# Optimization experiments

Measured on AMD Instinct MI355X. Metric: run time of the kernel, lower is better.

The kernel has to match this reference:

```python
import jax, jax.numpy as jnp
import numpy as np

T, N = 24, 2048
INPUT_DIM, HIDDEN, MEDIATE, SOCIAL, OUT_DIM = 2, 64, 128, 64, 2
N_SIZE = 2
CELL = 0.3
T_OBS, T_PRED = 9, 19
WIN = (N_SIZE + 1) ** 2  # (N_size+1)^2 = 9 window cells


def _social_pool(h, coords, mask):
    """Faithful social pooling for N_size=2, grid_cell_size=0.3.

    torch builds a dynamic grid, scatter-adds every agent's h into its cell,
    then gathers grid[int(x-R):int(x+R), int(y-R):int(y+R)] per agent.
    With R=0.3 and integer positions >= 4 (guaranteed by the margin), that
    slice is exactly the single cell (x-1, y-1), broadcast over the 3x3
    window. We compute it as a pairwise match without materializing a grid.
    Runs under torch.no_grad() -> stop_gradient.
    """
    margin = 2 * N_SIZE * CELL
    lt = jnp.stack([coords[:, 0].min(), coords[:, 1].min()]) - margin
    p = jnp.floor((coords - lt) / CELL).astype(jnp.int32)            # [N,2]
    p = p * mask.astype(jnp.int32)[:, None]                          # masked agents -> cell (0,0)
    q = p - 1                                                        # gathered cell per agent
    match = (p[None, :, 0] == q[:, None, 0]) & (p[None, :, 1] == q[:, None, 1])  # [i,j]
    cell_val = match.astype(h.dtype) @ h                             # [N,hidden] scatter-add + gather
    Hf = jnp.tile(cell_val, (1, WIN)) * mask[:, None]                # broadcast over 3x3 window, flat
    return jax.lax.stop_gradient(Hf)


def _forward(X, part_masks, all_h_t, all_c_t, Y, W_in, b_in, W_soc, b_soc,
             W_ih, W_hh, b_ih, b_hh, W_out, b_out, T_obs, T_pred):
    relu = jax.nn.relu  # dropout_prob = 0 -> Phi == ReLU

    def lstm(z, h, c):
        g = z @ W_ih.T + b_ih + h @ W_hh.T + b_hh
        i, f, gg, o = jnp.split(g, 4, axis=1)
        c = jax.nn.sigmoid(f) * c + jax.nn.sigmoid(i) * jnp.tanh(gg)
        h = jax.nn.sigmoid(o) * jnp.tanh(c)
        return h, c

    def cell_out(r, h, c, coords, m):
        Hf = _social_pool(h, coords, m)
        e = relu(Hf @ W_soc.T + b_soc)
        z = jnp.concatenate([r, e], axis=1)
        h, c = lstm(z, h, c)
        out = (h @ W_out.T + b_out) * m[:, None]
        return h, c, out

    def step_obs(carry, inp):
        h, c = carry
        x, m = inp
        r = relu(x @ W_in.T + b_in)
        h, c, out = cell_out(r, h, c, x, m)
        return (h, c), out

    (h, c), outs_obs = jax.lax.scan(
        step_obs, (all_h_t, all_c_t), (X[:T_obs + 1], part_masks[:T_obs + 1]))

    def step_pred(carry, inp):
        h, c, last_pt, prev_out = carry
        x, m = inp
        r = relu(last_pt @ W_in.T + b_in)
        h, c, out = cell_out(r, h, c, x, m)
        # torch: last_point = outputs[frame_idx - 1] AFTER the frame runs
        return (h, c, prev_out, out), out

    carry0 = (h, c, X[T_obs + 1], outs_obs[-1])
    _, outs_pred = jax.lax.scan(
        step_pred, carry0, (X[T_obs + 1:T_pred + 1], part_masks[T_obs + 1:T_pred + 1]))

    tail = jnp.zeros((X.shape[0] - T_pred - 1, X.shape[1], OUT_DIM), X.dtype)
    return jnp.concatenate([outs_obs, outs_pred, tail], axis=0)


def setup_inputs() -> dict:
    key = jax.random.key(0)
    ks = jax.random.split(key, 13)

    def lin(kw, kb, out_d, in_d):  # torch nn.Linear default init
        lim = 1.0 / float(np.sqrt(in_d))
        W = jax.random.uniform(kw, (out_d, in_d), minval=-lim, maxval=lim, dtype=jnp.float32)
        b = jax.random.uniform(kb, (out_d,), minval=-lim, maxval=lim, dtype=jnp.float32)
        return W, b

    W_in, b_in = lin(ks[0], ks[1], MEDIATE, INPUT_DIM)
    W_soc, b_soc = lin(ks[2], ks[3], SOCIAL, WIN * HIDDEN)
    W_ih, b_ih = lin(ks[4], ks[5], 4 * HIDDEN, MEDIATE + SOCIAL)
    W_hh, b_hh = lin(ks[6], ks[7], 4 * HIDDEN, HIDDEN)
    W_out, b_out = lin(ks[8], ks[9], OUT_DIM, HIDDEN)

    X = jax.random.normal(ks[10], (T, N, INPUT_DIM), dtype=jnp.float32) * 10.0  # meter-scale coords
    part_masks = (jax.random.uniform(ks[11], (T, N)) < 0.9).astype(jnp.float32)  # binary presence mask
    Y = jax.random.normal(ks[12], (T, N, INPUT_DIM), dtype=jnp.float32)  # unused by forward
    all_h_t = jnp.zeros((N, HIDDEN), jnp.float32)
    all_c_t = jnp.zeros((N, HIDDEN), jnp.float32)

    return {"X": X, "part_masks": part_masks, "all_h_t": all_h_t, "all_c_t": all_c_t,
            "Y": Y, "T_obs": T_OBS, "T_pred": T_PRED,
            "W_in": W_in, "b_in": b_in, "W_soc": W_soc, "b_soc": b_soc,
            "W_ih": W_ih, "W_hh": W_hh, "b_ih": b_ih, "b_hh": b_hh,
            "W_out": W_out, "b_out": b_out}


def reference(X, part_masks, all_h_t, all_c_t, Y, T_obs, T_pred,
              W_in, b_in, W_soc, b_soc, W_ih, W_hh, b_ih, b_hh, W_out, b_out):
    return _forward(X, part_masks, all_h_t, all_c_t, Y, W_in, b_in, W_soc, b_soc,
                    W_ih, W_hh, b_ih, b_hh, W_out, b_out, int(T_obs), int(T_pred))
```

## Files before the change

kernel.cpp:

```cpp
#include <hip/hip_runtime.h>
#include <math.h>


#define N_AG   2048
#define STEPS  20
#define CAP    12
#define NSRV   21
#define MAGIC  0x13572468

typedef short short8 __attribute__((ext_vector_type(8)));
typedef float f32x4  __attribute__((ext_vector_type(4)));
union FU { uint4 q; short8 v; };

__device__ __forceinline__ void pack8(const float* v, uint4& hq, uint4& lq) {
    unsigned uh[4], ul[4];
    #pragma unroll
    for (int w = 0; w < 4; w++) {
        float v0 = v[2 * w], v1 = v[2 * w + 1];
        unsigned h;
        asm("v_cvt_pk_bf16_f32 %0, %1, %2" : "=v"(h) : "v"(v0), "v"(v1));
        float f0 = __uint_as_float(h << 16);
        float f1 = __uint_as_float(h & 0xffff0000u);
        float r0 = v0 - f0, r1 = v1 - f1;
        unsigned l;
        asm("v_cvt_pk_bf16_f32 %0, %1, %2" : "=v"(l) : "v"(r0), "v"(r1));
        uh[w] = h; ul[w] = l;
    }
    hq = make_uint4(uh[0], uh[1], uh[2], uh[3]);
    lq = make_uint4(ul[0], ul[1], ul[2], ul[3]);
}

__device__ __forceinline__ int khash(int k) {
    return (int)(((unsigned)k * 2654435761u) >> 21);
}

__device__ __forceinline__ float fsigm(float x) {
    return __builtin_amdgcn_rcpf(1.f + __expf(-x));
}
__device__ __forceinline__ float ftanh(float x) {
    float e = __expf(2.f * x);
    return 1.f - 2.f * __builtin_amdgcn_rcpf(e + 1.f);
}

__device__ __forceinline__ void bar_lds() {
    asm volatile("s_waitcnt lgkmcnt(0)\n\ts_barrier" ::: "memory");
}

__device__ __forceinline__ void ast(int* p_, int v) {
    __hip_atomic_store(p_, v, __ATOMIC_RELAXED, __HIP_MEMORY_SCOPE_AGENT);
}
__device__ __forceinline__ void astf(float* p_, float v) {
    __hip_atomic_store(p_, v, __ATOMIC_RELAXED, __HIP_MEMORY_SCOPE_AGENT);
}
__device__ __forceinline__ unsigned long long aldu64(const unsigned long long* p_) {
    return __hip_atomic_load(p_, __ATOMIC_RELAXED, __HIP_MEMORY_SCOPE_AGENT);
}

struct KP {
    const float *X, *masks, *h_in, *c_in;
    const float *Win, *bin, *Wsoc, *bsoc, *Wih, *Whh, *bih, *bhh, *Wout, *bout;
    float *Wef;
    int *mcnt, *midx, *need, *flags;
    float *out;
    unsigned long long *hist;
};

__global__ __launch_bounds__(512, 1) void k_all(KP p)
{
    __shared__ __align__(16) uint4 zshq[544];
    __shared__ float gbuf[16][260];
    __shared__ float gbuf2[8][260];
    __shared__ __align__(16) float cvs[8][68];
    __shared__ __align__(16) float hs[8][68];
    __shared__ __align__(16) float sWefP[64 * 66];
    __shared__ float2 sWinP[16 * 17];
    __shared__ float sBinP[16 * 9];
    __shared__ float sX[11][8][2];
    __shared__ float sMask[STEPS][8];
    __shared__ int   sCnt[STEPS][8];
    __shared__ int   sNeed[19][8];
    __shared__ int   sMidx[STEPS][8][CAP];
    __shared__ float sBsoc[64], sBc[256], sWout[128], sBout[2];
    __shared__ uint4 sE0h[8], sE0l[8];
    __shared__ int kk[N_AG];
    __shared__ int head[N_AG];
    __shared__ int nxt[N_AG];
    __shared__ float red[512];

    const int tid = threadIdx.x;
    const int bxg = blockIdx.x;

    if (bxg < NSRV) {
        const int sb = bxg;
        {
            int lo = sb * 780;
            int hi = (sb == NSRV - 1) ? 16384 : lo + 780;
            for (int i = lo + tid; i < hi; i += 512)
                p.out[20 * N_AG * 2 + i] = 0.f;
        }
        if (sb == 20) {
            for (int i = tid; i < 4096; i += 512) {
                int s = i >> 6, k = i & 63;
                float a = 0.f;
                #pragma unroll
                for (int w = 0; w < 9; w++) a += p.Wsoc[s * 576 + w * 64 + k];
                astf(&p.Wef[i], a);
            }
            __syncthreads();
            if (tid == 0) ast(&p.flags[20], MAGIC);
        } else {
            const int t = sb;
            const float* Xt = p.X + t * N_AG * 2;

            float mnx = 1e30f, mny = 1e30f;
            for (int i = tid; i < N_AG; i += 512) {
                mnx = fminf(mnx, Xt[2 * i]);
                mny = fminf(mny, Xt[2 * i + 1]);
            }
            red[tid] = mnx; __syncthreads();
            for (int s = 256; s > 0; s >>= 1) { if (tid < s) red[tid] = fminf(red[tid], red[tid + s]); __syncthreads(); }
            float ltx = red[0]; __syncthreads();
            red[tid] = mny; __syncthreads();
            for (int s = 256; s > 0; s >>= 1) { if (tid < s) red[tid] = fminf(red[tid], red[tid + s]); __syncthreads(); }
            float lty = red[0]; __syncthreads();
            ltx -= 1.2f;
            lty -= 1.2f;

            for (int i = tid; i < N_AG; i += 512) {
                float m = p.masks[t * N_AG + i];
                int px = (int)floorf((Xt[2 * i]     - ltx) / 0.3f);
                int py = (int)floorf((Xt[2 * i + 1] - lty) / 0.3f);
                int im = (int)m;
                px *= im; py *= im;
                kk[i] = px * 65536 + py;
                head[i] = -1;
                if (t >= 1) ast(&p.need[(t - 1) * N_AG + i], 0);
            }
            __syncthreads();
            for (int j = tid; j < N_AG; j += 512) {
                int kj = kk[j];
                if (kj != 0) nxt[j] = atomicExch(&head[khash(kj)], j);
            }
            __syncthreads();
            for (int i = tid; i < N_AG; i += 512) {
                int ki = kk[i];
                int cnt = 0;
                int base = (t * N_AG + i) * CAP;
                if (ki != 0) {
                    int tkey = ki - 65537;
                    int lst[CAP];
                    for (int j = head[khash(tkey)]; j >= 0; j = nxt[j]) {
                        if (kk[j] == tkey) { if (cnt < CAP) lst[cnt] = j; cnt++; }
                    }
                    if (cnt > CAP) cnt = CAP;
                    for (int a = 1; a < cnt; a++) {
                        int v = lst[a]; int b = a - 1;
                        while (b >= 0 && lst[b] > v) { lst[b + 1] = lst[b]; b--; }
                        lst[b + 1] = v;
                    }
                    for (int a = 0; a < cnt; a++) {
                        ast(&p.midx[base + a], lst[a]);
                        if (t >= 1) ast(&p.need[(t - 1) * N_AG + lst[a]], 1);
                    }
                }
                ast(&p.mcnt[t * N_AG + i], cnt);
            }
            __syncthreads();
            if (tid == 0) ast(&p.flags[t], MAGIC);
        }
    }

    const int wbase = bxg * 8;
    const int wv    = tid >> 6, lane = tid & 63;
    const int mA    = lane & 15, quad = lane >> 4;
    const int nt0   = 2 * wv;
    const int w     = wv;

    if (tid < 256) sBc[tid] = p.bih[tid] + p.bhh[tid];
    if (tid < 128) {
        sWout[tid] = p.Wout[tid];
        int c = tid;
        sWinP[(c >> 3) * 17 + (c & 7)] = make_float2(p.Win[2 * c], p.Win[2 * c + 1]);
        sBinP[(c >> 3) * 9 + (c & 7)] = p.bin[c];
    }
    if (tid < 64) sBsoc[tid] = p.bsoc[tid];
    if (tid < 2)  sBout[tid] = p.bout[tid];
    if (tid < 8) {
        float v[8];
        #pragma unroll
        for (int j = 0; j < 8; j++) v[j] = fmaxf(p.bsoc[tid * 8 + j], 0.f);
        pack8(v, sE0h[tid], sE0l[tid]);
    }
    if (tid < 176) { int tt = tid / 16, r = tid % 16;
                     sX[tt][r >> 1][r & 1] = p.X[tt * (N_AG * 2) + (wbase + (r >> 1)) * 2 + (r & 1)]; }
    if (tid < 160) { int tt = tid / 8, m2 = tid % 8;
                     sMask[tt][m2] = p.masks[tt * N_AG + wbase + m2]; }

    float c0;
    {
        hs[w][lane] = p.h_in[(wbase + w) * 64 + lane];
        c0 = p.c_in[(wbase + w) * 64 + lane];
    }

    FU wh[2][8], wl[2][8];
    #pragma unroll
    for (int e = 0; e < 2; e++) {
        int g = (nt0 + e) * 16 + mA;
        #pragma unroll
        for (int kt = 0; kt < 8; kt++) {
            int k0 = kt * 32 + quad * 8;
            const float* src = (k0 < 192) ? (p.Wih + g * 192 + k0)
                                          : (p.Whh + g * 64 + (k0 - 192));
            float v[8];
            #pragma unroll
            for (int j = 0; j < 8; j++) v[j] = src[j];
            pack8(v, wh[e][kt].q, wl[e][kt].q);
        }
    }
    FU woh[2], wol[2];
    #pragma unroll
    for (int e2 = 0; e2 < 2; e2++) {
        int kt = 6 + e2;
        float v[8];
        #pragma unroll
        for (int j = 0; j < 8; j++) {
            int k0 = kt * 32 + quad * 8 + j - 192;
            v[j] = (mA < 2) ? p.Wout[mA * 64 + k0] : 0.f;
        }
        pack8(v, woh[e2].q, wol[e2].q);
    }

    if (tid < NSRV) {
        while (__hip_atomic_load(&p.flags[tid], __ATOMIC_RELAXED,
                                 __HIP_MEMORY_SCOPE_AGENT) != MAGIC) { }
    }
    __syncthreads();

    if (tid < 160) { int tt = tid / 8, m2 = tid % 8;
                     sCnt[tt][m2] = p.mcnt[tt * N_AG + wbase + m2]; }
    if (tid < 152) { int s = tid / 8, m2 = tid % 8;
                     sNeed[s][m2] = p.need[s * N_AG + wbase + m2]; }
    for (int i = tid; i < 4096; i += 512) sWefP[(i >> 6) * 66 + (i & 63)] = p.Wef[i];
    for (int i = tid; i < STEPS * 8 * CAP; i += 512) {
        int tt = i / (8 * CAP), r = i % (8 * CAP), m2 = r / CAP, n = r % CAP;
        sMidx[tt][m2][n] = p.midx[(tt * N_AG + wbase + m2) * CAP + n];
    }
    __syncthreads();

    {
        if (lane < 16) {
            float px = sX[0][w][0], py = sX[0][w][1];
            float v[8];
            #pragma unroll
            for (int j = 0; j < 8; j++) {
                float2 w2 = sWinP[lane * 17 + j];
                v[j] = fmaxf(w2.x * px + w2.y * py + sBinP[lane * 9 + j], 0.f);
            }
            pack8(v, zshq[lane * 17 + w], zshq[lane * 17 + w + 8]);
        } else if (lane < 24) {
            int s58 = lane - 16;
            const float4* hr = (const float4*)&hs[w][s58 * 8];
            float4 h0 = hr[0], h1 = hr[1];
            float v[8] = { h0.x, h0.y, h0.z, h0.w, h1.x, h1.y, h1.z, h1.w };
            pack8(v, zshq[(24 + s58) * 17 + w], zshq[(24 + s58) * 17 + w + 8]);
        } else if (lane < 32) {
            int s58 = lane - 24;
            if (sCnt[0][w] == 0) {
                zshq[(16 + s58) * 17 + w]     = sE0h[s58];
                zshq[(16 + s58) * 17 + w + 8] = sE0l[s58];
            }
        }
        int cnt0 = sCnt[0][w];
        if (cnt0 > 0) {
            float a = 0.f;
            for (int n = 0; n < cnt0; n++) {
                int r = sMidx[0][w][n];
                a += p.h_in[r * 64 + lane];
            }
            cvs[w][lane] = a;
            asm volatile("s_waitcnt lgkmcnt(0)" ::: "memory");
            float acc = sBsoc[lane], accb = 0.f;
            const float4* cw = (const float4*)&cvs[w][0];
            const float2* wq = (const float2*)&sWefP[lane * 66];
            #pragma unroll
            for (int k4 = 0; k4 < 16; k4++) {
                float4 ca = cw[k4];
                float2 wa = wq[2 * k4], wb = wq[2 * k4 + 1];
                acc  += ca.x * wa.x + ca.y * wa.y;
                accb += ca.z * wb.x + ca.w * wb.y;
            }
            acc = fmaxf(acc + accb, 0.f);
            float v[8];
            #pragma unroll
            for (int j = 0; j < 8; j++) v[j] = __shfl(acc, (lane & 7) * 8 + j, 64);
            if (lane < 8)
                pack8(v, zshq[(16 + lane) * 17 + w], zshq[(16 + lane) * 17 + w + 8]);
        }
    }
    bar_lds();

    #pragma unroll 1
    for (int t = 0; t < STEPS; t++) {
        f32x4 a0v = {0.f, 0.f, 0.f, 0.f};
        f32x4 a1v = {0.f, 0.f, 0.f, 0.f};
        f32x4 a0l = {0.f, 0.f, 0.f, 0.f};
        f32x4 a1l = {0.f, 0.f, 0.f, 0.f};
        f32x4 ovv = {0.f, 0.f, 0.f, 0.f};
        f32x4 ovl = {0.f, 0.f, 0.f, 0.f};
        #pragma unroll
        for (int kt = 0; kt < 8; kt++) {
            FU az;
            az.q = zshq[(kt * 4 + quad) * 17 + mA];
            a0v = __builtin_amdgcn_mfma_f32_16x16x32_bf16(az.v, wh[0][kt].v, a0v, 0, 0, 0);
            a1v = __builtin_amdgcn_mfma_f32_16x16x32_bf16(az.v, wh[1][kt].v, a1v, 0, 0, 0);
            a0l = __builtin_amdgcn_mfma_f32_16x16x32_bf16(az.v, wl[0][kt].v, a0l, 0, 0, 0);
            a1l = __builtin_amdgcn_mfma_f32_16x16x32_bf16(az.v, wl[1][kt].v, a1l, 0, 0, 0);
            if (kt >= 6 && wv == 0) {
                ovv = __builtin_amdgcn_mfma_f32_16x16x32_bf16(az.v, woh[kt - 6].v, ovv, 0, 0, 0);
                ovl = __builtin_amdgcn_mfma_f32_16x16x32_bf16(az.v, wol[kt - 6].v, ovl, 0, 0, 0);
            }
        }
        #pragma unroll
        for (int r = 0; r < 4; r++) {
            int row = quad * 4 + r;
            gbuf[row][nt0 * 16 + mA]       = a0v[r];
            gbuf[row][(nt0 + 1) * 16 + mA] = a1v[r];
        }
        if (quad < 2) {
            #pragma unroll
            for (int r = 0; r < 4; r++) {
                int row = quad * 4 + r;
                gbuf2[row][nt0 * 16 + mA]       = a0l[r];
                gbuf2[row][(nt0 + 1) * 16 + mA] = a1l[r];
            }
        }
        if (wv == 0 && mA < 2) {
            #pragma unroll
            for (int r = 0; r < 4; r++) {
                int row = quad * 4 + r;
                gbuf[row][256 + mA] = ovv[r];
                if (quad < 2) gbuf2[row][256 + mA] = ovl[r];
            }
        }
        bar_lds();

        {
            const int hid = lane;
            float gi = gbuf[w][hid]       + gbuf[w + 8][hid]       + gbuf2[w][hid]       + sBc[hid];
            float gf = gbuf[w][64 + hid]  + gbuf[w + 8][64 + hid]  + gbuf2[w][64 + hid]  + sBc[64 + hid];
            float gR = gbuf[w][128 + hid] + gbuf[w + 8][128 + hid] + gbuf2[w][128 + hid] + sBc[128 + hid];
            float go = gbuf[w][192 + hid] + gbuf[w + 8][192 + hid] + gbuf2[w][192 + hid] + sBc[192 + hid];
            float cn = fsigm(gf) * c0 + fsigm(gi) * ftanh(gR);
            float hn = fsigm(go) * ftanh(cn);
            c0 = cn;
            hs[w][hid] = hn;

            if (t <= 18 && sNeed[t][w]) {
                unsigned long long* hp = p.hist + (size_t)t * (N_AG * 64);
                unsigned long long tg = ((unsigned long long)(t + 1)) << 32;
                __hip_atomic_store(&hp[(wbase + w) * 64 + hid],
                                   tg | (unsigned long long)__float_as_uint(hn),
                                   __ATOMIC_RELAXED, __HIP_MEMORY_SCOPE_AGENT);
            }

            const unsigned long long* hb = p.hist + (size_t)t * (N_AG * 64);
            int cntN = 0, rfirst = -1, rsecond = -1;
            unsigned long long pw0 = 0, qw0 = 0;
            if (t < STEPS - 1) {
                cntN = sCnt[t + 1][w];
                if (cntN > 0) {
                    rfirst = sMidx[t + 1][w][0];
                    pw0 = aldu64(&hb[rfirst * 64 + lane]);
                    if (cntN > 1) {
                        rsecond = sMidx[t + 1][w][1];
                        qw0 = aldu64(&hb[rsecond * 64 + lane]);
                    }
                }
            }

            float q0 = 0.f, q1 = 0.f;
            if (t >= 1) {
                float mkp = sMask[t - 1][w];
                q0 = (gbuf[w][256] + gbuf[w + 8][256] + gbuf2[w][256] + sBout[0]) * mkp;
                q1 = (gbuf[w][257] + gbuf[w + 8][257] + gbuf2[w][257] + sBout[1]) * mkp;
                if (lane == 0)
                    *(float2*)&p.out[((t - 1) * N_AG + wbase + w) * 2] = make_float2(q0, q1);
            }
            if (t == STEPS - 1) {
                float p0 = hn * sWout[hid], p1 = hn * sWout[64 + hid];
                #pragma unroll
                for (int off = 32; off >= 1; off >>= 1) {
                    p0 += __shfl_xor(p0, off);
                    p1 += __shfl_xor(p1, off);
                }
                float mk = sMask[t][w];
                if (lane == 0)
                    *(float2*)&p.out[(t * N_AG + wbase + w) * 2] =
                        make_float2((p0 + sBout[0]) * mk, (p1 + sBout[1]) * mk);
            }

            if (t < STEPS - 1) {
                const int tn = t + 1;
                if (lane < 16) {
                    float px, py;
                    if (tn <= 10) { px = sX[tn][w][0]; py = sX[tn][w][1]; }
                    else          { px = q0; py = q1; }
                    float v[8];
                    #pragma unroll
                    for (int j = 0; j < 8; j++) {
                        float2 w2 = sWinP[lane * 17 + j];
                        v[j] = fmaxf(w2.x * px + w2.y * py + sBinP[lane * 9 + j], 0.f);
                    }
                    pack8(v, zshq[lane * 17 + w], zshq[lane * 17 + w + 8]);
                } else if (lane < 24) {
                    int s58 = lane - 16;
                    const float4* hr = (const float4*)&hs[w][s58 * 8];
                    float4 h0 = hr[0], h1 = hr[1];
                    float v[8] = { h0.x, h0.y, h0.z, h0.w, h1.x, h1.y, h1.z, h1.w };
                    pack8(v, zshq[(24 + s58) * 17 + w], zshq[(24 + s58) * 17 + w + 8]);
                } else if (lane < 32) {
                    int s58 = lane - 24;
                    if (sCnt[tn][w] == 0) {
                        zshq[(16 + s58) * 17 + w]     = sE0h[s58];
                        zshq[(16 + s58) * 17 + w + 8] = sE0l[s58];
                    }
                }
            }

            if (cntN > 0) {
                const unsigned tagw = (unsigned)(t + 1);
                while ((unsigned)(pw0 >> 32) != tagw)
                    pw0 = aldu64(&hb[rfirst * 64 + lane]);
                float a = __uint_as_float((unsigned)pw0);
                if (cntN > 1) {
                    while ((unsigned)(qw0 >> 32) != tagw)
                        qw0 = aldu64(&hb[rsecond * 64 + lane]);
                    a += __uint_as_float((unsigned)qw0);
                    for (int n = 2; n < cntN; n++) {
                        int r = sMidx[t + 1][w][n];
                        unsigned long long w0_;
                        do {
                            w0_ = aldu64(&hb[r * 64 + lane]);
                        } while ((unsigned)(w0_ >> 32) != tagw);
                        a += __uint_as_float((unsigned)w0_);
                    }
                }
                cvs[w][lane] = a;
                asm volatile("s_waitcnt lgkmcnt(0)" ::: "memory");
                float acc = sBsoc[lane], accb = 0.f;
                const float4* cw = (const float4*)&cvs[w][0];
                const float2* wq = (const float2*)&sWefP[lane * 66];
                #pragma unroll
                for (int k4 = 0; k4 < 16; k4++) {
                    float4 ca = cw[k4];
                    float2 wa = wq[2 * k4], wb = wq[2 * k4 + 1];
                    acc  += ca.x * wa.x + ca.y * wa.y;
                    accb += ca.z * wb.x + ca.w * wb.y;
                }
                acc = fmaxf(acc + accb, 0.f);
                float v[8];
                #pragma unroll
                for (int j = 0; j < 8; j++) v[j] = __shfl(acc, (lane & 7) * 8 + j, 64);
                if (lane < 8)
                    pack8(v, zshq[(16 + lane) * 17 + w], zshq[(16 + lane) * 17 + w + 8]);
            }
        }
        bar_lds();
    }
}

extern "C" void kernel_launch(void* const* d_in, const int* in_sizes, int n_in,
                              void* d_out, int out_size, void* d_ws, size_t ws_size,
                              hipStream_t stream)
{
    KP kp;
    kp.X     = (const float*)d_in[0];
    kp.masks = (const float*)d_in[1];
    kp.h_in  = (const float*)d_in[2];
    kp.c_in  = (const float*)d_in[3];
    kp.Win   = (const float*)d_in[7];
    kp.bin   = (const float*)d_in[8];
    kp.Wsoc  = (const float*)d_in[9];
    kp.bsoc  = (const float*)d_in[10];
    kp.Wih   = (const float*)d_in[11];
    kp.Whh   = (const float*)d_in[12];
    kp.bih   = (const float*)d_in[13];
    kp.bhh   = (const float*)d_in[14];
    kp.Wout  = (const float*)d_in[15];
    kp.bout  = (const float*)d_in[16];
    kp.out   = (float*)d_out;

    unsigned long long* hist = (unsigned long long*)d_ws;
    float* Wef  = (float*)(hist + 19 * N_AG * 64);
    int*   need = (int*)(Wef + 4096);
    int*   mcnt = need + 19 * N_AG;
    int*   midx = mcnt + STEPS * N_AG;
    int*   flags = midx + STEPS * N_AG * CAP;

    kp.hist = hist; kp.Wef = Wef; kp.need = need; kp.mcnt = mcnt;
    kp.midx = midx; kp.flags = flags;

    k_all<<<256, 512, 0, stream>>>(kp);
}
```

Before: 157.3 us.

## Add warp-specialized waves for output projection and social-pool gathering

Raises the block from 512 to 768 threads and gives the extra waves their own jobs. Wave 8 computes the output projection MFMA, and waves 8-11 spin on the cross-block hidden-state history and compute the social embedding, while waves 0-7 do only the LSTM gate MFMAs and cell update. The per-step critical path of the LSTM waves should shrink, since they no longer wait on remote hidden states or the extra output MFMAs. The server blocks' min reductions now use wavefront shuffles instead of a shared-memory tree. In exchange there is more register and scheduling pressure from the larger block, and the gather waves poll without an early prefetch, so they may serialize differently.

After: 192.1 us. 22.1% more time.

```diff
diff --git a/kernel.cpp b/kernel.cpp
--- a/kernel.cpp
+++ b/kernel.cpp
@@ -7,6 +7,7 @@
 #define CAP    12
 #define NSRV   21
 #define MAGIC  0x13572468
+#define NTHR   768
 
 typedef short short8 __attribute__((ext_vector_type(8)));
 typedef float f32x4  __attribute__((ext_vector_type(4)));
@@ -65,7 +66,7 @@
     unsigned long long *hist;
 };
 
-__global__ __launch_bounds__(512, 1) void k_all(KP p)
+__global__ __launch_bounds__(NTHR, 1) void k_all(KP p)
 {
     __shared__ __align__(16) uint4 zshq[544];
     __shared__ float gbuf[16][260];
@@ -85,7 +86,7 @@
     __shared__ int kk[N_AG];
     __shared__ int head[N_AG];
     __shared__ int nxt[N_AG];
-    __shared__ float red[512];
+    __shared__ float red[128];
 
     const int tid = threadIdx.x;
     const int bxg = blockIdx.x;
@@ -95,11 +96,11 @@
         {
             int lo = sb * 780;
             int hi = (sb == NSRV - 1) ? 16384 : lo + 780;
-            for (int i = lo + tid; i < hi; i += 512)
+            for (int i = lo + tid; i < hi; i += NTHR)
                 p.out[20 * N_AG * 2 + i] = 0.f;
         }
         if (sb == 20) {
-            for (int i = tid; i < 4096; i += 512) {
+            for (int i = tid; i < 4096; i += NTHR) {
                 int s = i >> 6, k = i & 63;
                 float a = 0.f;
                 #pragma unroll
@@ -113,20 +114,29 @@
             const float* Xt = p.X + t * N_AG * 2;
 
             float mnx = 1e30f, mny = 1e30f;
-            for (int i = tid; i < N_AG; i += 512) {
+            for (int i = tid; i < N_AG; i += NTHR) {
                 mnx = fminf(mnx, Xt[2 * i]);
                 mny = fminf(mny, Xt[2 * i + 1]);
             }
-            red[tid] = mnx; __syncthreads();
-            for (int s = 256; s > 0; s >>= 1) { if (tid < s) red[tid] = fminf(red[tid], red[tid + s]); __syncthreads(); }
-            float ltx = red[0]; __syncthreads();
-            red[tid] = mny; __syncthreads();
-            for (int s = 256; s > 0; s >>= 1) { if (tid < s) red[tid] = fminf(red[tid], red[tid + s]); __syncthreads(); }
-            float lty = red[0]; __syncthreads();
-            ltx -= 1.2f;
-            lty -= 1.2f;
-
-            for (int i = tid; i < N_AG; i += 512) {
+            #pragma unroll
+            for (int off = 32; off >= 1; off >>= 1) {
+                mnx = fminf(mnx, __shfl_xor(mnx, off));
+                mny = fminf(mny, __shfl_xor(mny, off));
+            }
+            if ((tid & 63) == 0) { red[tid >> 6] = mnx; red[32 + (tid >> 6)] = mny; }
+            __syncthreads();
+            if (tid == 0) {
+                float ax = red[0], ay = red[32];
+                for (int u = 1; u < NTHR / 64; u++) {
+                    ax = fminf(ax, red[u]); ay = fminf(ay, red[32 + u]);
+                }
+                red[64] = ax; red[65] = ay;
+            }
+            __syncthreads();
+            float ltx = red[64] - 1.2f;
+            float lty = red[65] - 1.2f;
+
+            for (int i = tid; i < N_AG; i += NTHR) {
                 float m = p.masks[t * N_AG + i];
                 int px = (int)floorf((Xt[2 * i]     - ltx) / 0.3f);
                 int py = (int)floorf((Xt[2 * i + 1] - lty) / 0.3f);
@@ -137,12 +147,12 @@
                 if (t >= 1) ast(&p.need[(t - 1) * N_AG + i], 0);
             }
             __syncthreads();
-            for (int j = tid; j < N_AG; j += 512) {
+            for (int j = tid; j < N_AG; j += NTHR) {
                 int kj = kk[j];
                 if (kj != 0) nxt[j] = atomicExch(&head[khash(kj)], j);
             }
             __syncthreads();
-            for (int i = tid; i < N_AG; i += 512) {
+            for (int i = tid; i < N_AG; i += NTHR) {
                 int ki = kk[i];
                 int cnt = 0;
                 int base = (t * N_AG + i) * CAP;
@@ -196,38 +206,42 @@
     if (tid < 160) { int tt = tid / 8, m2 = tid % 8;
                      sMask[tt][m2] = p.masks[tt * N_AG + wbase + m2]; }
 
-    float c0;
-    {
+    float c0 = 0.f;
+    if (wv < 8) {
         hs[w][lane] = p.h_in[(wbase + w) * 64 + lane];
         c0 = p.c_in[(wbase + w) * 64 + lane];
     }
 
     FU wh[2][8], wl[2][8];
-    #pragma unroll
-    for (int e = 0; e < 2; e++) {
-        int g = (nt0 + e) * 16 + mA;
+    if (wv < 8) {
         #pragma unroll
-        for (int kt = 0; kt < 8; kt++) {
-            int k0 = kt * 32 + quad * 8;
-            const float* src = (k0 < 192) ? (p.Wih + g * 192 + k0)
-                                          : (p.Whh + g * 64 + (k0 - 192));
+        for (int e = 0; e < 2; e++) {
+            int g = (nt0 + e) * 16 + mA;
+            #pragma unroll
+            for (int kt = 0; kt < 8; kt++) {
+                int k0 = kt * 32 + quad * 8;
+                const float* src = (k0 < 192) ? (p.Wih + g * 192 + k0)
+                                              : (p.Whh + g * 64 + (k0 - 192));
+                float v[8];
+                #pragma unroll
+                for (int j = 0; j < 8; j++) v[j] = src[j];
+                pack8(v, wh[e][kt].q, wl[e][kt].q);
+            }
+        }
+    }
+    FU woh[2], wol[2];
+    if (wv == 8) {
+        #pragma unroll
+        for (int e2 = 0; e2 < 2; e2++) {
+            int kt = 6 + e2;
             float v[8];
             #pragma unroll
-            for (int j = 0; j < 8; j++) v[j] = src[j];
-            pack8(v, wh[e][kt].q, wl[e][kt].q);
-        }
-    }
-    FU woh[2], wol[2];
-    #pragma unroll
-    for (int e2 = 0; e2 < 2; e2++) {
-        int kt = 6 + e2;
-        float v[8];
-        #pragma unroll
-        for (int j = 0; j < 8; j++) {
-            int k0 = kt * 32 + quad * 8 + j - 192;
-            v[j] = (mA < 2) ? p.Wout[mA * 64 + k0] : 0.f;
-        }
-        pack8(v, woh[e2].q, wol[e2].q);
+            for (int j = 0; j < 8; j++) {
+                int k0 = kt * 32 + quad * 8 + j - 192;
+                v[j] = (mA < 2) ? p.Wout[mA * 64 + k0] : 0.f;
+            }
+            pack8(v, woh[e2].q, wol[e2].q);
+        }
     }
 
     if (tid < NSRV) {
@@ -240,14 +254,14 @@
                      sCnt[tt][m2] = p.mcnt[tt * N_AG + wbase + m2]; }
     if (tid < 152) { int s = tid / 8, m2 = tid % 8;
                      sNeed[s][m2] = p.need[s * N_AG + wbase + m2]; }
-    for (int i = tid; i < 4096; i += 512) sWefP[(i >> 6) * 66 + (i & 63)] = p.Wef[i];
-    for (int i = tid; i < STEPS * 8 * CAP; i += 512) {
+    for (int i = tid; i < 4096; i += NTHR) sWefP[(i >> 6) * 66 + (i & 63)] = p.Wef[i];
+    for (int i = tid; i < STEPS * 8 * CAP; i += NTHR) {
         int tt = i / (8 * CAP), r = i % (8 * CAP), m2 = r / CAP, n = r % CAP;
         sMidx[tt][m2][n] = p.midx[(tt * N_AG + wbase + m2) * CAP + n];
     }
     __syncthreads();
 
-    {
+    if (wv < 8) {
         if (lane < 16) {
             float px = sX[0][w][0], py = sX[0][w][1];
             float v[8];
@@ -301,50 +315,57 @@
 
     #pragma unroll 1
     for (int t = 0; t < STEPS; t++) {
-        f32x4 a0v = {0.f, 0.f, 0.f, 0.f};
-        f32x4 a1v = {0.f, 0.f, 0.f, 0.f};
-        f32x4 a0l = {0.f, 0.f, 0.f, 0.f};
-        f32x4 a1l = {0.f, 0.f, 0.f, 0.f};
-        f32x4 ovv = {0.f, 0.f, 0.f, 0.f};
-        f32x4 ovl = {0.f, 0.f, 0.f, 0.f};
-        #pragma unroll
-        for (int kt = 0; kt < 8; kt++) {
-            FU az;
-            az.q = zshq[(kt * 4 + quad) * 17 + mA];
-            a0v = __builtin_amdgcn_mfma_f32_16x16x32_bf16(az.v, wh[0][kt].v, a0v, 0, 0, 0);
-            a1v = __builtin_amdgcn_mfma_f32_16x16x32_bf16(az.v, wh[1][kt].v, a1v, 0, 0, 0);
-            a0l = __builtin_amdgcn_mfma_f32_16x16x32_bf16(az.v, wl[0][kt].v, a0l, 0, 0, 0);
-            a1l = __builtin_amdgcn_mfma_f32_16x16x32_bf16(az.v, wl[1][kt].v, a1l, 0, 0, 0);
-            if (kt >= 6 && wv == 0) {
-                ovv = __builtin_amdgcn_mfma_f32_16x16x32_bf16(az.v, woh[kt - 6].v, ovv, 0, 0, 0);
-                ovl = __builtin_amdgcn_mfma_f32_16x16x32_bf16(az.v, wol[kt - 6].v, ovl, 0, 0, 0);
-            }
-        }
-        #pragma unroll
-        for (int r = 0; r < 4; r++) {
-            int row = quad * 4 + r;
-            gbuf[row][nt0 * 16 + mA]       = a0v[r];
-            gbuf[row][(nt0 + 1) * 16 + mA] = a1v[r];
-        }
-        if (quad < 2) {
+        if (wv < 8) {
+            f32x4 a0v = {0.f, 0.f, 0.f, 0.f};
+            f32x4 a1v = {0.f, 0.f, 0.f, 0.f};
+            f32x4 a0l = {0.f, 0.f, 0.f, 0.f};
+            f32x4 a1l = {0.f, 0.f, 0.f, 0.f};
+            #pragma unroll
+            for (int kt = 0; kt < 8; kt++) {
+                FU az;
+                az.q = zshq[(kt * 4 + quad) * 17 + mA];
+                a0v = __builtin_amdgcn_mfma_f32_16x16x32_bf16(az.v, wh[0][kt].v, a0v, 0, 0, 0);
+                a1v = __builtin_amdgcn_mfma_f32_16x16x32_bf16(az.v, wh[1][kt].v, a1v, 0, 0, 0);
+                a0l = __builtin_amdgcn_mfma_f32_16x16x32_bf16(az.v, wl[0][kt].v, a0l, 0, 0, 0);
+                a1l = __builtin_amdgcn_mfma_f32_16x16x32_bf16(az.v, wl[1][kt].v, a1l, 0, 0, 0);
+            }
             #pragma unroll
             for (int r = 0; r < 4; r++) {
                 int row = quad * 4 + r;
-                gbuf2[row][nt0 * 16 + mA]       = a0l[r];
-                gbuf2[row][(nt0 + 1) * 16 + mA] = a1l[r];
-            }
-        }
-        if (wv == 0 && mA < 2) {
-            #pragma unroll
-            for (int r = 0; r < 4; r++) {
-                int row = quad * 4 + r;
-                gbuf[row][256 + mA] = ovv[r];
-                if (quad < 2) gbuf2[row][256 + mA] = ovl[r];
+                gbuf[row][nt0 * 16 + mA]       = a0v[r];
+                gbuf[row][(nt0 + 1) * 16 + mA] = a1v[r];
+            }
+            if (quad < 2) {
+                #pragma unroll
+                for (int r = 0; r < 4; r++) {
+                    int row = quad * 4 + r;
+                    gbuf2[row][nt0 * 16 + mA]       = a0l[r];
+                    gbuf2[row][(nt0 + 1) * 16 + mA] = a1l[r];
+                }
+            }
+        } else if (wv == 8) {
+            f32x4 ovv = {0.f, 0.f, 0.f, 0.f};
+            f32x4 ovl = {0.f, 0.f, 0.f, 0.f};
+            #pragma unroll
+            for (int e2 = 0; e2 < 2; e2++) {
+                int kt = 6 + e2;
+                FU az;
+                az.q = zshq[(kt * 4 + quad) * 17 + mA];
+                ovv = __builtin_amdgcn_mfma_f32_16x16x32_bf16(az.v, woh[e2].v, ovv, 0, 0, 0);
+                ovl = __builtin_amdgcn_mfma_f32_16x16x32_bf16(az.v, wol[e2].v, ovl, 0, 0, 0);
+            }
+            if (mA < 2) {
+                #pragma unroll
+                for (int r = 0; r < 4; r++) {
+                    int row = quad * 4 + r;
+                    gbuf[row][256 + mA] = ovv[r];
+                    if (quad < 2) gbuf2[row][256 + mA] = ovl[r];
+                }
             }
         }
         bar_lds();
 
-        {
+        if (wv < 8) {
             const int hid = lane;
             float gi = gbuf[w][hid]       + gbuf[w + 8][hid]       + gbuf2[w][hid]       + sBc[hid];
             float gf = gbuf[w][64 + hid]  + gbuf[w + 8][64 + hid]  + gbuf2[w][64 + hid]  + sBc[64 + hid];
@@ -361,21 +382,6 @@
                 __hip_atomic_store(&hp[(wbase + w) * 64 + hid],
                                    tg | (unsigned long long)__float_as_uint(hn),
                                    __ATOMIC_RELAXED, __HIP_MEMORY_SCOPE_AGENT);
-            }
-
-            const unsigned long long* hb = p.hist + (size_t)t * (N_AG * 64);
-            int cntN = 0, rfirst = -1, rsecond = -1;
-            unsigned long long pw0 = 0, qw0 = 0;
-            if (t < STEPS - 1) {
-                cntN = sCnt[t + 1][w];
-                if (cntN > 0) {
-                    rfirst = sMidx[t + 1][w][0];
-                    pw0 = aldu64(&hb[rfirst * 64 + lane]);
-                    if (cntN > 1) {
-                        rsecond = sMidx[t + 1][w][1];
-                        qw0 = aldu64(&hb[rsecond * 64 + lane]);
-                    }
-                }
             }
 
             float q0 = 0.f, q1 = 0.f;
@@ -418,51 +424,53 @@
                     float4 h0 = hr[0], h1 = hr[1];
                     float v[8] = { h0.x, h0.y, h0.z, h0.w, h1.x, h1.y, h1.z, h1.w };
                     pack8(v, zshq[(24 + s58) * 17 + w], zshq[(24 + s58) * 17 + w + 8]);
-                } else if (lane < 32) {
-                    int s58 = lane - 24;
-                    if (sCnt[tn][w] == 0) {
-                        zshq[(16 + s58) * 17 + w]     = sE0h[s58];
-                        zshq[(16 + s58) * 17 + w + 8] = sE0l[s58];
-                    }
-                }
-            }
-
-            if (cntN > 0) {
-                const unsigned tagw = (unsigned)(t + 1);
-                while ((unsigned)(pw0 >> 32) != tagw)
-                    pw0 = aldu64(&hb[rfirst * 64 + lane]);
-                float a = __uint_as_float((unsigned)pw0);
-                if (cntN > 1) {
-                    while ((unsigned)(qw0 >> 32) != tagw)
-                        qw0 = aldu64(&hb[rsecond * 64 + lane]);
-                    a += __uint_as_float((unsigned)qw0);
-                    for (int n = 2; n < cntN; n++) {
-                        int r = sMidx[t + 1][w][n];
+                }
+            }
+        } else if (t < STEPS - 1) {
+            const int hw = wv - 8;
+            const unsigned long long* hb = p.hist + (size_t)t * (N_AG * 64);
+            const unsigned tagw = (unsigned)(t + 1);
+            #pragma unroll
+            for (int k = 0; k < 2; k++) {
+                const int ag = hw * 2 + k;
+                int cntN = sCnt[t + 1][ag];
+                if (cntN == 0) {
+                    if (lane < 8) {
+                        zshq[(16 + lane) * 17 + ag]     = sE0h[lane];
+                        zshq[(16 + lane) * 17 + ag + 8] = sE0l[lane];
+                    }
+                } else {
+                    int rfirst = sMidx[t + 1][ag][0];
+                    unsigned long long pw0 = aldu64(&hb[rfirst * 64 + lane]);
+                    while ((unsigned)(pw0 >> 32) != tagw)
+                        pw0 = aldu64(&hb[rfirst * 64 + lane]);
+                    float a = __uint_as_float((unsigned)pw0);
+                    for (int n = 1; n < cntN; n++) {
+                        int r = sMidx[t + 1][ag][n];
                         unsigned long long w0_;
-                        do {
-                            w0_ = aldu64(&hb[r * 64 + lane]);
-                        } while ((unsigned)(w0_ >> 32) != tagw);
+                        do { w0_ = aldu64(&hb[r * 64 + lane]); }
+                        while ((unsigned)(w0_ >> 32) != tagw);
                         a += __uint_as_float((unsigned)w0_);
                     }
-                }
-                cvs[w][lane] = a;
-                asm volatile("s_waitcnt lgkmcnt(0)" ::: "memory");
-                float acc = sBsoc[lane], accb = 0.f;
-                const float4* cw = (const float4*)&cvs[w][0];
-                const float2* wq = (const float2*)&sWefP[lane * 66];
-                #pragma unroll
-                for (int k4 = 0; k4 < 16; k4++) {
-                    float4 ca = cw[k4];
-                    float2 wa = wq[2 * k4], wb = wq[2 * k4 + 1];
-                    acc  += ca.x * wa.x + ca.y * wa.y;
-                    accb += ca.z * wb.x + ca.w * wb.y;
-                }
-                acc = fmaxf(acc + accb, 0.f);
-                float v[8];
-                #pragma unroll
-                for (int j = 0; j < 8; j++) v[j] = __shfl(acc, (lane & 7) * 8 + j, 64);
-                if (lane < 8)
-                    pack8(v, zshq[(16 + lane) * 17 + w], zshq[(16 + lane) * 17 + w + 8]);
+                    cvs[ag][lane] = a;
+                    asm volatile("s_waitcnt lgkmcnt(0)" ::: "memory");
+                    float acc = sBsoc[lane], accb = 0.f;
+                    const float4* cw = (const float4*)&cvs[ag][0];
+                    const float2* wq = (const float2*)&sWefP[lane * 66];
+                    #pragma unroll
+                    for (int k4 = 0; k4 < 16; k4++) {
+                        float4 ca = cw[k4];
+                        float2 wa = wq[2 * k4], wb = wq[2 * k4 + 1];
+                        acc  += ca.x * wa.x + ca.y * wa.y;
+                        accb += ca.z * wb.x + ca.w * wb.y;
+                    }
+                    acc = fmaxf(acc + accb, 0.f);
+                    float v[8];
+                    #pragma unroll
+                    for (int j = 0; j < 8; j++) v[j] = __shfl(acc, (lane & 7) * 8 + j, 64);
+                    if (lane < 8)
+                        pack8(v, zshq[(16 + lane) * 17 + ag], zshq[(16 + lane) * 17 + ag + 8]);
+                }
             }
         }
         bar_lds();
@@ -500,5 +508,5 @@
     kp.hist = hist; kp.Wef = Wef; kp.need = need; kp.mcnt = mcnt;
     kp.midx = midx; kp.flags = flags;
 
-    k_all<<<256, 512, 0, stream>>>(kp);
-}
+    k_all<<<256, NTHR, 0, stream>>>(kp);
+}
```
